# Optimization experiments

Measured on AMD Instinct MI355X. Metric: run time of the kernel, lower is better.

## Reference

```python
import jax, jax.numpy as jnp
import numpy as np

HIDDEN = 1024
HEADS = 16
HEAD_DIM = HIDDEN // HEADS
EPS = 1e-6


def _layernorm(x, gamma, beta):
    mu = jnp.mean(x, axis=-1, keepdims=True)
    var = jnp.mean(jnp.square(x - mu), axis=-1, keepdims=True)
    return (x - mu) * jax.lax.rsqrt(var + EPS) * gamma + beta


def setup_inputs() -> dict:
    key = jax.random.key(0)
    ks = jax.random.split(key, 16)
    B, S, D = 2, 2048, HIDDEN
    s = 1.0 / np.sqrt(D)
    inp = {
        "x": jax.random.normal(ks[0], (B, S, D), dtype=jnp.float32),
        "Wq": jax.random.uniform(ks[1], (D, D), jnp.float32, -s, s),
        "bq": jnp.zeros((D,), jnp.float32),
        "Wk": jax.random.uniform(ks[2], (D, D), jnp.float32, -s, s),
        "bk": jnp.zeros((D,), jnp.float32),
        "Wv": jax.random.uniform(ks[3], (D, D), jnp.float32, -s, s),
        "bv": jnp.zeros((D,), jnp.float32),
        "Wo": jax.random.uniform(ks[4], (D, D), jnp.float32, -s, s),
        "bo": jnp.zeros((D,), jnp.float32),
        "g1": jnp.ones((D,), jnp.float32),
        "b1": jnp.zeros((D,), jnp.float32),
        "Wup": jax.random.uniform(ks[5], (D, 4 * D), jnp.float32, -s, s),
        "bup": jnp.zeros((4 * D,), jnp.float32),
        "Wdn": jax.random.uniform(ks[6], (4 * D, D), jnp.float32, -0.5 * s, 0.5 * s),
        "bdn": jnp.zeros((D,), jnp.float32),
        "g2": jnp.ones((D,), jnp.float32),
        "b2": jnp.zeros((D,), jnp.float32),
    }
    return inp


def _forward(x, Wq, bq, Wk, bk, Wv, bv, Wo, bo, g1, b1, Wup, bup, Wdn, bdn, g2, b2):
    B, S, D = x.shape
    H, Hd = HEADS, HEAD_DIM
    # projections -> (B, H, S, Hd)
    q = (x @ Wq + bq).reshape(B, S, H, Hd).transpose(0, 2, 1, 3)
    k = (x @ Wk + bk).reshape(B, S, H, Hd).transpose(0, 2, 1, 3)
    v = (x @ Wv + bv).reshape(B, S, H, Hd).transpose(0, 2, 1, 3)
    # full NxN scores (faithful to the source: explicit QK^T, mask, softmax, AV)
    scores = jnp.einsum("bhqd,bhkd->bhqk", q, k) / np.sqrt(Hd)
    causal = jnp.tril(jnp.ones((S, S), dtype=bool))  # (S, S)
    scores = jnp.where(causal, scores, jnp.float32(-1e20))
    attn = jax.nn.softmax(scores, axis=-1)
    # dropout is identity in eval mode
    mid = jnp.einsum("bhqk,bhkd->bqhd", attn, v).reshape(B, S, D)
    attn_out = mid @ Wo + bo
    x = _layernorm(x + attn_out, g1, b1)
    # FFN
    up = jax.nn.relu(x @ Wup + bup)
    down = up @ Wdn + bdn
    return _layernorm(x + down, g2, b2)


def reference(x, Wq, bq, Wk, bk, Wv, bv, Wo, bo, g1, b1, Wup, bup, Wdn, bdn, g2, b2):
    return _forward(x, Wq, bq, Wk, bk, Wv, bv, Wo, bo, g1, b1, Wup, bup, Wdn, bdn, g2, b2)
```

## Files before the change

kernel.cpp:

```cpp
#include <hip/hip_runtime.h>

#define D_MODEL 1024
#define D_FFN   4096
#define SEQ     2048
#define NROWS   4096
#define QKV_LD  3072

typedef __bf16 bf16x8 __attribute__((ext_vector_type(8)));
typedef float  floatx4 __attribute__((ext_vector_type(4)));

#define MFMA_BF16 __builtin_amdgcn_mfma_f32_16x16x32_bf16

__device__ __forceinline__ unsigned short f2bf(float f) {
  unsigned int u = __float_as_uint(f);
  u += 0x7FFFu + ((u >> 16) & 1u);
  return (unsigned short)(u >> 16);
}

template <int C>
__device__ __forceinline__ float ror16(float x) {
  return __int_as_float(
      __builtin_amdgcn_mov_dpp(__float_as_int(x), 0x120 | C, 0xf, 0xf, true));
}

__device__ __forceinline__ void async16(const unsigned short* g, unsigned short* l) {
  __builtin_amdgcn_global_load_lds(
      (const __attribute__((address_space(1))) unsigned int*)g,
      (__attribute__((address_space(3))) unsigned int*)l, 16, 0, 0);
}

__global__ __launch_bounds__(256) void k_f32_to_bf16(
    const float* __restrict__ in, unsigned short* __restrict__ outp, long n) {
  long i = ((long)blockIdx.x * 256 + threadIdx.x) * 4;
  if (i >= n) return;
  float4 v = *(const float4*)(in + i);
  ushort4 o;
  o.x = f2bf(v.x); o.y = f2bf(v.y); o.z = f2bf(v.z); o.w = f2bf(v.w);
  *(ushort4*)(outp + i) = o;
}

__global__ __launch_bounds__(256) void k_transpose_bf16(
    const float* __restrict__ W, unsigned short* __restrict__ WT, int R, int C) {
  __shared__ float tile[32][33];
  int tx = threadIdx.x & 31, ty = threadIdx.x >> 5;
  long bx = (long)blockIdx.x * 32;
  long by = (long)blockIdx.y * 32;
  #pragma unroll
  for (int j = 0; j < 4; j++)
    tile[ty + j * 8][tx] = W[(by + ty + j * 8) * C + bx + tx];
  __syncthreads();
  #pragma unroll
  for (int j = 0; j < 4; j++)
    WT[(bx + ty + j * 8) * R + by + tx] = f2bf(tile[tx][ty + j * 8]);
}

__global__ __launch_bounds__(256) void k_transpose_sq(
    const float* __restrict__ Wq, const float* __restrict__ Wk,
    const float* __restrict__ Wv, const float* __restrict__ Wo,
    unsigned short* __restrict__ WqkvT, unsigned short* __restrict__ WoT) {
  __shared__ float tile[32][33];
  int z = blockIdx.z;
  const float* W = (z == 0) ? Wq : (z == 1) ? Wk : (z == 2) ? Wv : Wo;
  unsigned short* dst = (z < 3) ? (WqkvT + (size_t)z * D_MODEL * D_MODEL) : WoT;
  int tx = threadIdx.x & 31, ty = threadIdx.x >> 5;
  long bx = (long)blockIdx.x * 32;
  long by = (long)blockIdx.y * 32;
  #pragma unroll
  for (int j = 0; j < 4; j++)
    tile[ty + j * 8][tx] = W[(by + ty + j * 8) * D_MODEL + bx + tx];
  __syncthreads();
  #pragma unroll
  for (int j = 0; j < 4; j++)
    dst[(bx + ty + j * 8) * D_MODEL + by + tx] = f2bf(tile[tx][ty + j * 8]);
}

__global__ __launch_bounds__(256) void k_pack_bias(
    const float* __restrict__ bq, const float* __restrict__ bk,
    const float* __restrict__ bv, float* __restrict__ dst) {
  int i = blockIdx.x * 256 + threadIdx.x;
  if (i >= 3072) return;
  float v = (i < 1024) ? bq[i] : (i < 2048) ? bk[i - 1024] : bv[i - 2048];
  dst[i] = v;
}

__global__ __launch_bounds__(256) void k_transpose_v(
    const unsigned short* __restrict__ QKV, unsigned short* __restrict__ Vt) {
  __shared__ unsigned short tile[64][72];
  int r0 = blockIdx.x * 64;
  int c0 = blockIdx.y * 64;
  int tx = threadIdx.x & 15, ty = threadIdx.x >> 4;
  #pragma unroll
  for (int j = 0; j < 4; j++) {
    int r = ty + j * 16;
    *(ushort4*)&tile[r][tx * 4] =
        *(const ushort4*)(QKV + (long)(r0 + r) * QKV_LD + 2048 + c0 + tx * 4);
  }
  __syncthreads();
  #pragma unroll
  for (int j = 0; j < 4; j++) {
    int d = ty + j * 16;
    ushort4 o;
    o.x = tile[tx * 4 + 0][d];
    o.y = tile[tx * 4 + 1][d];
    o.z = tile[tx * 4 + 2][d];
    o.w = tile[tx * 4 + 3][d];
    *(ushort4*)(Vt + (long)(c0 + d) * NROWS + r0 + tx * 4) = o;
  }
}

__global__ __launch_bounds__(512, 4) void k_gemm128(
    const unsigned short* __restrict__ A,
    const unsigned short* __restrict__ Bt,
    const float* __restrict__ bias,
    void* __restrict__ Cp, int M, int N, int K, int flags, int rx, int ry) {
  __shared__ unsigned short lds[2 * 16384];
  int tid = threadIdx.x, lane = tid & 63, wave = tid >> 6;
  int quad = lane >> 4, l16 = lane & 15;
  int wm = wave >> 2, wn = wave & 3;

  int nx = gridDim.x, ny = gridDim.y;
  int orig = blockIdx.y * nx + blockIdx.x;
  int xcd = orig & 7;
  int s = orig >> 3;
  int mr = nx / rx, mc = ny / ry;
  int rr = xcd / ry, rc = xcd % ry;
  int im = s % mr, in_ = s / mr;
  long bm = (long)(rr * mr + im) * 128;
  long bn = (long)(rc * mc + in_) * 128;

  int T = K / 64;

  const floatx4 fz = {0.f, 0.f, 0.f, 0.f};
  floatx4 acc[4][2];
  #pragma unroll
  for (int i = 0; i < 4; i++)
    #pragma unroll
    for (int j = 0; j < 2; j++) acc[i][j] = fz;

  int srow = tid >> 3;
  int sc = (tid & 7) ^ (srow & 7);
  const unsigned short* Ag = A + (bm + srow) * (long)K + sc * 8;
  const unsigned short* Bg = Bt + (bn + srow) * (long)K + sc * 8;

  auto stage = [&](int tt, int c) {
    unsigned short* An = lds + c * 16384;
    unsigned short* Bn = An + 8192;
    long ko = (long)tt * 64;
    async16(Ag + ko, An + wave * 512);
    async16(Ag + 64 * (long)K + ko, An + 4096 + wave * 512);
    async16(Bg + ko, Bn + wave * 512);
    async16(Bg + 64 * (long)K + ko, Bn + 4096 + wave * 512);
  };

  int aoff = (wm * 64 + l16) * 64;
  int boff = (wn * 32 + l16) * 64;
  int sw = l16 & 7;
  int ca0 = (quad ^ sw) * 8;
  int ca1 = ((4 + quad) ^ sw) * 8;

  stage(0, 0);
  for (int t = 0; t < T; t++) {
    int c = t & 1;
    const unsigned short* Ac = lds + c * 16384;
    const unsigned short* Bc = Ac + 8192;
    int tn = (t + 1 < T) ? t + 1 : T - 1;
    stage(tn, c ^ 1);
    __asm__ volatile("s_waitcnt vmcnt(4)" ::: "memory");
    __builtin_amdgcn_s_barrier();

    bf16x8 af[4][2], bfr[2][2];
    #pragma unroll
    for (int m = 0; m < 4; m++) {
      af[m][0] = *(const bf16x8*)(Ac + aoff + m * 1024 + ca0);
      af[m][1] = *(const bf16x8*)(Ac + aoff + m * 1024 + ca1);
    }
    #pragma unroll
    for (int n = 0; n < 2; n++) {
      bfr[n][0] = *(const bf16x8*)(Bc + boff + n * 1024 + ca0);
      bfr[n][1] = *(const bf16x8*)(Bc + boff + n * 1024 + ca1);
    }
    __asm__ volatile("s_waitcnt lgkmcnt(0)" ::: "memory");
    __builtin_amdgcn_s_setprio(1);
    #pragma unroll
    for (int h = 0; h < 2; h++)
      #pragma unroll
      for (int m = 0; m < 4; m++)
        #pragma unroll
        for (int n = 0; n < 2; n++)
          acc[m][n] = MFMA_BF16(af[m][h], bfr[n][h], acc[m][n], 0, 0, 0);
    __builtin_amdgcn_s_setprio(0);
    __builtin_amdgcn_s_barrier();
  }

  bool f32out = (flags & 1) != 0;
  bool relu   = (flags & 2) != 0;
  if (f32out) {
    float* outf = (float*)Cp;
    #pragma unroll
    for (int n = 0; n < 2; n++) {
      long col = bn + wn * 32 + n * 16 + l16;
      float bvv = bias[col];
      #pragma unroll
      for (int m = 0; m < 4; m++) {
        long row = bm + wm * 64 + m * 16 + quad * 4;
        #pragma unroll
        for (int r = 0; r < 4; r++) {
          float v = acc[m][n][r] + bvv;
          if (relu) v = fmaxf(v, 0.0f);
          outf[(row + r) * (long)N + col] = v;
        }
      }
    }
  } else {
    __asm__ volatile("s_waitcnt vmcnt(0)" ::: "memory");
    __syncthreads();
    unsigned short* outh = (unsigned short*)Cp;
    unsigned short* lw = lds + wave * 2560;
    #pragma unroll
    for (int n = 0; n < 2; n++) {
      long col = bn + wn * 32 + n * 16 + l16;
      float bvv = bias[col];
      #pragma unroll
      for (int m = 0; m < 4; m++) {
        #pragma unroll
        for (int r = 0; r < 4; r++) {
          float v = acc[m][n][r] + bvv;
          if (relu) v = fmaxf(v, 0.0f);
          lw[(m * 16 + quad * 4 + r) * 40 + n * 16 + l16] = f2bf(v);
        }
      }
    }
    int rrb = lane >> 2;
    int c8 = (lane & 3) * 8;
    long grow = bm + wm * 64;
    long gcol = bn + wn * 32 + c8;
    #pragma unroll
    for (int k = 0; k < 4; k++) {
      int rw = rrb + k * 16;
      bf16x8 vv = *(const bf16x8*)(lw + rw * 40 + c8);
      *(bf16x8*)(outh + (grow + rw) * (long)N + gcol) = vv;
    }
  }
}

#define PLD 72
__global__ __launch_bounds__(256) void k_attn(
    const unsigned short* __restrict__ QKV,
    const unsigned short* __restrict__ Vt,
    unsigned short* __restrict__ Omat) {
  __shared__ unsigned short Ks[64 * 64];
  __shared__ unsigned short Vs[64 * 64];
  __shared__ unsigned short Ps[4][16 * PLD];
  int tid = threadIdx.x;
  int lane = tid & 63, wave = tid >> 6;
  int quad = lane >> 4, l16 = lane & 15;
  int z = blockIdx.x;
  int bh = z & 31;
  int qt = 31 - (z >> 5);
  int b = bh >> 4, h = bh & 15;
  long rowbase = (long)b * SEQ;
  int hd0 = h * 64;
  unsigned short* pw = &Ps[wave][0];
  const float SCL = 0.18033688f;
  const floatx4 fz = {0.f, 0.f, 0.f, 0.f};

  int r_in = lane >> 3;
  int cpos = lane & 7;

  bf16x8 ones;
  #pragma unroll
  for (int i = 0; i < 8; i++) ones[i] = (__bf16)1.0f;

  int q0w = qt * 64 + wave * 16;
  int qrow = q0w + quad * 4;
  int ntiles = qt + 1;

  bf16x8 qf0, qf1;
  {
    const unsigned short* qp_ =
        QKV + (rowbase + q0w + l16) * (long)QKV_LD + hd0 + quad * 8;
    qf0 = *(const bf16x8*)(qp_);
    qf1 = *(const bf16x8*)(qp_ + 32);
  }

  floatx4 ao[4], aol;
  #pragma unroll
  for (int t = 0; t < 4; t++) ao[t] = fz;
  aol = fz;
  float m_i[4];
  #pragma unroll
  for (int r = 0; r < 4; r++) m_i[r] = -3.0e38f;

  for (int it = 0; it < ntiles; it++) {
    int kv0 = it << 6;
    #pragma unroll
    for (int jj = 0; jj < 2; jj++) {
      int j = wave * 2 + jj;
      int r = j * 8 + r_in;
      int c = cpos ^ (r & 7);
      const unsigned short* gk =
          QKV + (rowbase + kv0 + r) * (long)QKV_LD + 1024 + hd0 + c * 8;
      async16(gk, Ks + j * 512);
      const unsigned short* gv =
          Vt + (long)(hd0 + r) * NROWS + rowbase + kv0 + c * 8;
      async16(gv, Vs + j * 512);
    }
    __syncthreads();

    floatx4 sacc[4];
    #pragma unroll
    for (int t = 0; t < 4; t++) {
      int row = t * 16 + l16;
      int sw = row & 7;
      bf16x8 kf0 = *(const bf16x8*)(Ks + row * 64 + (quad ^ sw) * 8);
      bf16x8 kf1 = *(const bf16x8*)(Ks + row * 64 + ((quad + 4) ^ sw) * 8);
      sacc[t] = __builtin_amdgcn_mfma_f32_16x16x32_bf16(qf0, kf0, fz, 0, 0, 0);
      sacc[t] = __builtin_amdgcn_mfma_f32_16x16x32_bf16(qf1, kf1, sacc[t], 0, 0, 0);
    }

    if (it == ntiles - 1) {
      #pragma unroll
      for (int t = 0; t < 4; t++) {
        int kvc = kv0 + t * 16 + l16;
        #pragma unroll
        for (int r = 0; r < 4; r++)
          sacc[t][r] = (kvc > qrow + r) ? -1.0e30f : sacc[t][r];
      }
    }

    float Mg = sacc[0][0];
    #pragma unroll
    for (int t = 0; t < 4; t++)
      #pragma unroll
      for (int r = 0; r < 4; r++) Mg = fmaxf(Mg, sacc[t][r]);
    Mg = fmaxf(Mg, ror16<1>(Mg));
    Mg = fmaxf(Mg, ror16<2>(Mg));
    Mg = fmaxf(Mg, ror16<4>(Mg));
    Mg = fmaxf(Mg, ror16<8>(Mg));
    float Mg_s = Mg * SCL;

    float m_min = fminf(fminf(m_i[0], m_i[1]), fminf(m_i[2], m_i[3]));
    if (Mg_s > m_min + 8.0f) {
      #pragma unroll
      for (int r = 0; r < 4; r++) {
        float mn = fmaxf(m_i[r], Mg_s);
        float alpha = __builtin_amdgcn_exp2f(m_i[r] - mn);
        m_i[r] = mn;
        #pragma unroll
        for (int t = 0; t < 4; t++) ao[t][r] *= alpha;
        aol[r] *= alpha;
      }
    }

    #pragma unroll
    for (int t = 0; t < 4; t++)
      #pragma unroll
      for (int r = 0; r < 4; r++) {
        float p = __builtin_amdgcn_exp2f(fmaf(sacc[t][r], SCL, -m_i[r]));
        pw[(quad * 4 + r) * PLD + t * 16 + l16] =
            (unsigned short)(__float_as_uint(p) >> 16);
      }

    __asm__ volatile("s_waitcnt lgkmcnt(0)" ::: "memory");
    bf16x8 pf0 = *(const bf16x8*)(pw + l16 * PLD + quad * 8);
    bf16x8 pf1 = *(const bf16x8*)(pw + l16 * PLD + 32 + quad * 8);

    #pragma unroll
    for (int t = 0; t < 4; t++) {
      int row = t * 16 + l16;
      int sw = row & 7;
      bf16x8 vf0 = *(const bf16x8*)(Vs + row * 64 + (quad ^ sw) * 8);
      bf16x8 vf1 = *(const bf16x8*)(Vs + row * 64 + ((quad + 4) ^ sw) * 8);
      ao[t] = __builtin_amdgcn_mfma_f32_16x16x32_bf16(pf0, vf0, ao[t], 0, 0, 0);
      ao[t] = __builtin_amdgcn_mfma_f32_16x16x32_bf16(pf1, vf1, ao[t], 0, 0, 0);
    }
    aol = __builtin_amdgcn_mfma_f32_16x16x32_bf16(pf0, ones, aol, 0, 0, 0);
    aol = __builtin_amdgcn_mfma_f32_16x16x32_bf16(pf1, ones, aol, 0, 0, 0);

    __syncthreads();
  }

  float inv[4];
  #pragma unroll
  for (int r = 0; r < 4; r++) inv[r] = 1.0f / aol[r];
  #pragma unroll
  for (int t = 0; t < 4; t++)
    #pragma unroll
    for (int r = 0; r < 4; r++)
      Omat[(rowbase + qrow + r) * (long)D_MODEL + hd0 + t * 16 + l16] =
          f2bf(ao[t][r] * inv[r]);
}

__global__ __launch_bounds__(256) void k_add_ln(
    const float* __restrict__ A, const float* __restrict__ P,
    const float* __restrict__ g, const float* __restrict__ be,
    float* __restrict__ Y, unsigned short* __restrict__ Ybf) {
  __shared__ float sb[4], ssb[4];
  int tid = threadIdx.x;
  long base = (long)blockIdx.x * D_MODEL + tid * 4;
  float4 a  = *(const float4*)(A + base);
  float4 p0 = *(const float4*)(P + base);
  float v0 = a.x + p0.x;
  float v1 = a.y + p0.y;
  float v2 = a.z + p0.z;
  float v3 = a.w + p0.w;
  float s  = v0 + v1 + v2 + v3;
  float ss = v0 * v0 + v1 * v1 + v2 * v2 + v3 * v3;
  #pragma unroll
  for (int o = 32; o >= 1; o >>= 1) {
    s  += __shfl_xor(s, o, 64);
    ss += __shfl_xor(ss, o, 64);
  }
  int wave = tid >> 6;
  if ((tid & 63) == 0) { sb[wave] = s; ssb[wave] = ss; }
  __syncthreads();
  s  = sb[0] + sb[1] + sb[2] + sb[3];
  ss = ssb[0] + ssb[1] + ssb[2] + ssb[3];
  float mu  = s * (1.0f / 1024.0f);
  float var = ss * (1.0f / 1024.0f) - mu * mu;
  float rstd = rsqrtf(var + 1e-6f);
  float4 gv  = *(const float4*)(g + tid * 4);
  float4 bev = *(const float4*)(be + tid * 4);
  float o0 = (v0 - mu) * rstd * gv.x + bev.x;
  float o1 = (v1 - mu) * rstd * gv.y + bev.y;
  float o2 = (v2 - mu) * rstd * gv.z + bev.z;
  float o3 = (v3 - mu) * rstd * gv.w + bev.w;
  if (Y) *(float4*)(Y + base) = make_float4(o0, o1, o2, o3);
  if (Ybf) {
    ushort4 u;
    u.x = f2bf(o0); u.y = f2bf(o1); u.z = f2bf(o2); u.w = f2bf(o3);
    *(ushort4*)(Ybf + base) = u;
  }
}

extern "C" void kernel_launch(void* const* d_in, const int* in_sizes, int n_in,
                              void* d_out, int out_size, void* d_ws, size_t ws_size,
                              hipStream_t stream) {
  (void)in_sizes; (void)n_in; (void)out_size; (void)ws_size;
  const float* x   = (const float*)d_in[0];
  const float* Wq  = (const float*)d_in[1];
  const float* bq  = (const float*)d_in[2];
  const float* Wk  = (const float*)d_in[3];
  const float* bk  = (const float*)d_in[4];
  const float* Wv  = (const float*)d_in[5];
  const float* bv  = (const float*)d_in[6];
  const float* Wo  = (const float*)d_in[7];
  const float* bo  = (const float*)d_in[8];
  const float* g1  = (const float*)d_in[9];
  const float* b1  = (const float*)d_in[10];
  const float* Wup = (const float*)d_in[11];
  const float* bup = (const float*)d_in[12];
  const float* Wdn = (const float*)d_in[13];
  const float* bdn = (const float*)d_in[14];
  const float* g2  = (const float*)d_in[15];
  const float* b2  = (const float*)d_in[16];
  float* out = (float*)d_out;

  char* ws = (char*)d_ws;
  size_t off = 0;
  auto alloc = [&](size_t bytes) {
    char* p = ws + off;
    off = (off + bytes + 255) & ~(size_t)255;
    return p;
  };
  unsigned short* x_bf   = (unsigned short*)alloc((size_t)NROWS * D_MODEL * 2);
  unsigned short* WqkvT  = (unsigned short*)alloc((size_t)QKV_LD * D_MODEL * 2);
  unsigned short* WoT    = (unsigned short*)alloc((size_t)D_MODEL * D_MODEL * 2);
  unsigned short* WupT   = (unsigned short*)alloc((size_t)D_FFN * D_MODEL * 2);
  unsigned short* WdnT   = (unsigned short*)alloc((size_t)D_MODEL * D_FFN * 2);
  float*          bqkv   = (float*)alloc((size_t)QKV_LD * 4);
  unsigned short* qkv_bf = (unsigned short*)alloc((size_t)NROWS * QKV_LD * 2);
  unsigned short* Vt     = (unsigned short*)alloc((size_t)D_MODEL * NROWS * 2);
  unsigned short* mid_bf = (unsigned short*)alloc((size_t)NROWS * D_MODEL * 2);
  float*          x1f    = (float*)alloc((size_t)NROWS * D_MODEL * 4);
  unsigned short* x1bf   = (unsigned short*)alloc((size_t)NROWS * D_MODEL * 2);
  float*          part   = (float*)alloc((size_t)NROWS * D_MODEL * 4);
  unsigned short* h_bf   = (unsigned short*)alloc((size_t)NROWS * D_FFN * 2);

  k_f32_to_bf16<<<4096, 256, 0, stream>>>(x, x_bf, (long)NROWS * D_MODEL);
  k_transpose_sq<<<dim3(32, 32, 4), 256, 0, stream>>>(Wq, Wk, Wv, Wo, WqkvT, WoT);
  k_transpose_bf16<<<dim3(128, 32), 256, 0, stream>>>(Wup, WupT, D_MODEL, D_FFN);
  k_transpose_bf16<<<dim3(32, 128), 256, 0, stream>>>(Wdn, WdnT, D_FFN, D_MODEL);
  k_pack_bias<<<12, 256, 0, stream>>>(bq, bk, bv, bqkv);

  k_gemm128<<<dim3(32, 24), 512, 0, stream>>>(x_bf, WqkvT, bqkv, qkv_bf,
                                              NROWS, QKV_LD, D_MODEL, 0, 4, 2);
  k_transpose_v<<<dim3(64, 16), 256, 0, stream>>>(qkv_bf, Vt);

  k_attn<<<1024, 256, 0, stream>>>(qkv_bf, Vt, mid_bf);

  k_gemm128<<<dim3(32, 8), 512, 0, stream>>>(mid_bf, WoT, bo, part,
                                             NROWS, D_MODEL, D_MODEL, 1, 4, 2);
  k_add_ln<<<4096, 256, 0, stream>>>(x, part, g1, b1, x1f, x1bf);

  k_gemm128<<<dim3(32, 32), 512, 0, stream>>>(x1bf, WupT, bup, h_bf,
                                              NROWS, D_FFN, D_MODEL, 2, 4, 2);
  k_gemm128<<<dim3(32, 8), 512, 0, stream>>>(h_bf, WdnT, bdn, part,
                                             NROWS, D_MODEL, D_FFN, 1, 4, 2);
  k_add_ln<<<4096, 256, 0, stream>>>(x1f, part, g2, b2, out, nullptr);
}
```

Measured before the change: 343.8 us.

## Fuse prep kernels, write transposed V from QKV GEMM epilogue

```diff
diff --git a/kernel.cpp b/kernel.cpp
--- a/kernel.cpp
+++ b/kernel.cpp
@@ -29,90 +29,64 @@
       (__attribute__((address_space(3))) unsigned int*)l, 16, 0, 0);
 }
 
-__global__ __launch_bounds__(256) void k_f32_to_bf16(
-    const float* __restrict__ in, unsigned short* __restrict__ outp, long n) {
-  long i = ((long)blockIdx.x * 256 + threadIdx.x) * 4;
-  if (i >= n) return;
-  float4 v = *(const float4*)(in + i);
-  ushort4 o;
-  o.x = f2bf(v.x); o.y = f2bf(v.y); o.z = f2bf(v.z); o.w = f2bf(v.w);
-  *(ushort4*)(outp + i) = o;
-}
-
-__global__ __launch_bounds__(256) void k_transpose_bf16(
-    const float* __restrict__ W, unsigned short* __restrict__ WT, int R, int C) {
-  __shared__ float tile[32][33];
-  int tx = threadIdx.x & 31, ty = threadIdx.x >> 5;
-  long bx = (long)blockIdx.x * 32;
-  long by = (long)blockIdx.y * 32;
-  #pragma unroll
-  for (int j = 0; j < 4; j++)
-    tile[ty + j * 8][tx] = W[(by + ty + j * 8) * C + bx + tx];
-  __syncthreads();
-  #pragma unroll
-  for (int j = 0; j < 4; j++)
-    WT[(bx + ty + j * 8) * R + by + tx] = f2bf(tile[tx][ty + j * 8]);
-}
-
-__global__ __launch_bounds__(256) void k_transpose_sq(
+__global__ __launch_bounds__(256) void k_prep(
+    const float* __restrict__ x,
     const float* __restrict__ Wq, const float* __restrict__ Wk,
     const float* __restrict__ Wv, const float* __restrict__ Wo,
-    unsigned short* __restrict__ WqkvT, unsigned short* __restrict__ WoT) {
+    const float* __restrict__ Wup, const float* __restrict__ Wdn,
+    const float* __restrict__ bq, const float* __restrict__ bk,
+    const float* __restrict__ bv,
+    unsigned short* __restrict__ x_bf, unsigned short* __restrict__ WqkvT,
+    unsigned short* __restrict__ WoT, unsigned short* __restrict__ WupT,
+    unsigned short* __restrict__ WdnT, float* __restrict__ bqkv) {
   __shared__ float tile[32][33];
-  int z = blockIdx.z;
-  const float* W = (z == 0) ? Wq : (z == 1) ? Wk : (z == 2) ? Wv : Wo;
-  unsigned short* dst = (z < 3) ? (WqkvT + (size_t)z * D_MODEL * D_MODEL) : WoT;
+  int b = blockIdx.x;
+  if (b < 4096) {
+    long i = ((long)b * 256 + threadIdx.x) * 4;
+    float4 v = *(const float4*)(x + i);
+    ushort4 o;
+    o.x = f2bf(v.x); o.y = f2bf(v.y); o.z = f2bf(v.z); o.w = f2bf(v.w);
+    *(ushort4*)(x_bf + i) = o;
+    return;
+  }
+  if (b >= 16384) {
+    int i = (b - 16384) * 256 + threadIdx.x;
+    if (i < 3072) {
+      float v = (i < 1024) ? bq[i] : (i < 2048) ? bk[i - 1024] : bv[i - 2048];
+      bqkv[i] = v;
+    }
+    return;
+  }
+  const float* W; unsigned short* WT; int R, C, bx, by;
+  if (b < 8192) {
+    int z = (b - 4096) >> 10, idx = (b - 4096) & 1023;
+    W = (z == 0) ? Wq : (z == 1) ? Wk : (z == 2) ? Wv : Wo;
+    WT = (z < 3) ? (WqkvT + (size_t)z * D_MODEL * D_MODEL) : WoT;
+    R = D_MODEL; C = D_MODEL; bx = idx & 31; by = idx >> 5;
+  } else if (b < 12288) {
+    int idx = b - 8192;
+    W = Wup; WT = WupT; R = D_MODEL; C = D_FFN; bx = idx & 127; by = idx >> 7;
+  } else {
+    int idx = b - 12288;
+    W = Wdn; WT = WdnT; R = D_FFN; C = D_MODEL; bx = idx & 31; by = idx >> 5;
+  }
   int tx = threadIdx.x & 31, ty = threadIdx.x >> 5;
-  long bx = (long)blockIdx.x * 32;
-  long by = (long)blockIdx.y * 32;
+  long gx = (long)bx * 32, gy = (long)by * 32;
   #pragma unroll
   for (int j = 0; j < 4; j++)
-    tile[ty + j * 8][tx] = W[(by + ty + j * 8) * D_MODEL + bx + tx];
+    tile[ty + j * 8][tx] = W[(gy + ty + j * 8) * C + gx + tx];
   __syncthreads();
   #pragma unroll
   for (int j = 0; j < 4; j++)
-    dst[(bx + ty + j * 8) * D_MODEL + by + tx] = f2bf(tile[tx][ty + j * 8]);
-}
-
-__global__ __launch_bounds__(256) void k_pack_bias(
-    const float* __restrict__ bq, const float* __restrict__ bk,
-    const float* __restrict__ bv, float* __restrict__ dst) {
-  int i = blockIdx.x * 256 + threadIdx.x;
-  if (i >= 3072) return;
-  float v = (i < 1024) ? bq[i] : (i < 2048) ? bk[i - 1024] : bv[i - 2048];
-  dst[i] = v;
-}
-
-__global__ __launch_bounds__(256) void k_transpose_v(
-    const unsigned short* __restrict__ QKV, unsigned short* __restrict__ Vt) {
-  __shared__ unsigned short tile[64][72];
-  int r0 = blockIdx.x * 64;
-  int c0 = blockIdx.y * 64;
-  int tx = threadIdx.x & 15, ty = threadIdx.x >> 4;
-  #pragma unroll
-  for (int j = 0; j < 4; j++) {
-    int r = ty + j * 16;
-    *(ushort4*)&tile[r][tx * 4] =
-        *(const ushort4*)(QKV + (long)(r0 + r) * QKV_LD + 2048 + c0 + tx * 4);
-  }
-  __syncthreads();
-  #pragma unroll
-  for (int j = 0; j < 4; j++) {
-    int d = ty + j * 16;
-    ushort4 o;
-    o.x = tile[tx * 4 + 0][d];
-    o.y = tile[tx * 4 + 1][d];
-    o.z = tile[tx * 4 + 2][d];
-    o.w = tile[tx * 4 + 3][d];
-    *(ushort4*)(Vt + (long)(c0 + d) * NROWS + r0 + tx * 4) = o;
-  }
-}
-
-__global__ __launch_bounds__(512, 4) void k_gemm128(
+    WT[(gx + ty + j * 8) * R + gy + tx] = f2bf(tile[tx][ty + j * 8]);
+}
+
+__global__ __launch_bounds__(512, 2) void k_gemm128(
     const unsigned short* __restrict__ A,
     const unsigned short* __restrict__ Bt,
     const float* __restrict__ bias,
-    void* __restrict__ Cp, int M, int N, int K, int flags, int rx, int ry) {
+    void* __restrict__ Cp, unsigned short* __restrict__ VtOut,
+    int M, int N, int K, int flags, int rx, int ry) {
   __shared__ unsigned short lds[2 * 16384];
   int tid = threadIdx.x, lane = tid & 63, wave = tid >> 6;
   int quad = lane >> 4, l16 = lane & 15;
@@ -168,32 +142,31 @@
     __asm__ volatile("s_waitcnt vmcnt(4)" ::: "memory");
     __builtin_amdgcn_s_barrier();
 
-    bf16x8 af[4][2], bfr[2][2];
-    #pragma unroll
-    for (int m = 0; m < 4; m++) {
-      af[m][0] = *(const bf16x8*)(Ac + aoff + m * 1024 + ca0);
-      af[m][1] = *(const bf16x8*)(Ac + aoff + m * 1024 + ca1);
-    }
-    #pragma unroll
-    for (int n = 0; n < 2; n++) {
-      bfr[n][0] = *(const bf16x8*)(Bc + boff + n * 1024 + ca0);
-      bfr[n][1] = *(const bf16x8*)(Bc + boff + n * 1024 + ca1);
-    }
-    __asm__ volatile("s_waitcnt lgkmcnt(0)" ::: "memory");
-    __builtin_amdgcn_s_setprio(1);
-    #pragma unroll
-    for (int h = 0; h < 2; h++)
-      #pragma unroll
-      for (int m = 0; m < 4; m++)
-        #pragma unroll
-        for (int n = 0; n < 2; n++)
-          acc[m][n] = MFMA_BF16(af[m][h], bfr[n][h], acc[m][n], 0, 0, 0);
-    __builtin_amdgcn_s_setprio(0);
+    bf16x8 af0[4], bf0[2], af1[4], bf1[2];
+    #pragma unroll
+    for (int m = 0; m < 4; m++) af0[m] = *(const bf16x8*)(Ac + aoff + m * 1024 + ca0);
+    #pragma unroll
+    for (int n = 0; n < 2; n++) bf0[n] = *(const bf16x8*)(Bc + boff + n * 1024 + ca0);
+    #pragma unroll
+    for (int m = 0; m < 4; m++) af1[m] = *(const bf16x8*)(Ac + aoff + m * 1024 + ca1);
+    #pragma unroll
+    for (int n = 0; n < 2; n++) bf1[n] = *(const bf16x8*)(Bc + boff + n * 1024 + ca1);
+    #pragma unroll
+    for (int m = 0; m < 4; m++)
+      #pragma unroll
+      for (int n = 0; n < 2; n++)
+        acc[m][n] = MFMA_BF16(af0[m], bf0[n], acc[m][n], 0, 0, 0);
+    #pragma unroll
+    for (int m = 0; m < 4; m++)
+      #pragma unroll
+      for (int n = 0; n < 2; n++)
+        acc[m][n] = MFMA_BF16(af1[m], bf1[n], acc[m][n], 0, 0, 0);
     __builtin_amdgcn_s_barrier();
   }
 
   bool f32out = (flags & 1) != 0;
   bool relu   = (flags & 2) != 0;
+  bool vtr    = (flags & 4) != 0 && bn >= 2048;
   if (f32out) {
     float* outf = (float*)Cp;
     #pragma unroll
@@ -210,6 +183,34 @@
           outf[(row + r) * (long)N + col] = v;
         }
       }
+    }
+  } else if (vtr) {
+    __asm__ volatile("s_waitcnt vmcnt(0)" ::: "memory");
+    __syncthreads();
+    unsigned short* lwT = lds + wave * 2304;
+    #pragma unroll
+    for (int n = 0; n < 2; n++) {
+      long col = bn + wn * 32 + n * 16 + l16;
+      float bvv = bias[col];
+      ushort4 u;
+      #pragma unroll
+      for (int m = 0; m < 4; m++) {
+        u.x = f2bf(acc[m][0 + n][0] + bvv);
+        u.y = f2bf(acc[m][n][1] + bvv);
+        u.z = f2bf(acc[m][n][2] + bvv);
+        u.w = f2bf(acc[m][n][3] + bvv);
+        *(ushort4*)(lwT + (n * 16 + l16) * 72 + m * 16 + quad * 4) = u;
+      }
+    }
+    __syncthreads();
+    long d0 = bn - 2048 + wn * 32;
+    long grow = bm + wm * 64;
+    int rseg = (lane & 7) * 8;
+    #pragma unroll
+    for (int k = 0; k < 4; k++) {
+      int cl = k * 8 + (lane >> 3);
+      bf16x8 vv = *(const bf16x8*)(lwT + cl * 72 + rseg);
+      *(bf16x8*)(VtOut + (d0 + cl) * (long)NROWS + grow + rseg) = vv;
     }
   } else {
     __asm__ volatile("s_waitcnt vmcnt(0)" ::: "memory");
@@ -477,25 +478,21 @@
   float*          part   = (float*)alloc((size_t)NROWS * D_MODEL * 4);
   unsigned short* h_bf   = (unsigned short*)alloc((size_t)NROWS * D_FFN * 2);
 
-  k_f32_to_bf16<<<4096, 256, 0, stream>>>(x, x_bf, (long)NROWS * D_MODEL);
-  k_transpose_sq<<<dim3(32, 32, 4), 256, 0, stream>>>(Wq, Wk, Wv, Wo, WqkvT, WoT);
-  k_transpose_bf16<<<dim3(128, 32), 256, 0, stream>>>(Wup, WupT, D_MODEL, D_FFN);
-  k_transpose_bf16<<<dim3(32, 128), 256, 0, stream>>>(Wdn, WdnT, D_FFN, D_MODEL);
-  k_pack_bias<<<12, 256, 0, stream>>>(bq, bk, bv, bqkv);
-
-  k_gemm128<<<dim3(32, 24), 512, 0, stream>>>(x_bf, WqkvT, bqkv, qkv_bf,
-                                              NROWS, QKV_LD, D_MODEL, 0, 4, 2);
-  k_transpose_v<<<dim3(64, 16), 256, 0, stream>>>(qkv_bf, Vt);
+  k_prep<<<16396, 256, 0, stream>>>(x, Wq, Wk, Wv, Wo, Wup, Wdn, bq, bk, bv,
+                                    x_bf, WqkvT, WoT, WupT, WdnT, bqkv);
+
+  k_gemm128<<<dim3(32, 24), 512, 0, stream>>>(x_bf, WqkvT, bqkv, qkv_bf, Vt,
+                                              NROWS, QKV_LD, D_MODEL, 4, 4, 2);
 
   k_attn<<<1024, 256, 0, stream>>>(qkv_bf, Vt, mid_bf);
 
-  k_gemm128<<<dim3(32, 8), 512, 0, stream>>>(mid_bf, WoT, bo, part,
+  k_gemm128<<<dim3(32, 8), 512, 0, stream>>>(mid_bf, WoT, bo, part, nullptr,
                                              NROWS, D_MODEL, D_MODEL, 1, 4, 2);
   k_add_ln<<<4096, 256, 0, stream>>>(x, part, g1, b1, x1f, x1bf);
 
-  k_gemm128<<<dim3(32, 32), 512, 0, stream>>>(x1bf, WupT, bup, h_bf,
+  k_gemm128<<<dim3(32, 32), 512, 0, stream>>>(x1bf, WupT, bup, h_bf, nullptr,
                                               NROWS, D_FFN, D_MODEL, 2, 4, 2);
-  k_gemm128<<<dim3(32, 8), 512, 0, stream>>>(h_bf, WdnT, bdn, part,
+  k_gemm128<<<dim3(32, 8), 512, 0, stream>>>(h_bf, WdnT, bdn, part, nullptr,
                                              NROWS, D_MODEL, D_FFN, 1, 4, 2);
   k_add_ln<<<4096, 256, 0, stream>>>(x1f, part, g2, b2, out, nullptr);
 }
```

New measurement: 318.7 us. 7.3% less time.
